# Performance work log

Measured on AMD Instinct MI355X. Metric: run time of the kernel, lower is better.

Reference implementation:

```python
import jax, jax.numpy as jnp
import numpy as np

SIGMA = 1.0  # init kwarg: Gaussian kernel width

B, P, F = 8192, 8192, 256


def setup_inputs() -> dict:
    key = jax.random.key(0)
    kx, kp = jax.random.split(key)
    x = jax.random.normal(kx, (B, F), dtype=jnp.float32)
    prototypes = jax.random.normal(kp, (P, F), dtype=jnp.float32)
    return {"x": x, "prototypes": prototypes}


def reference(x, prototypes):
    x_sq = jnp.sum(x * x, axis=-1, keepdims=True)            # [B,1]
    p_sq = jnp.sum(prototypes * prototypes, axis=-1)          # [P]
    cross = jnp.einsum('bf,pf->bp', x, prototypes)            # [B,P]
    d2 = jnp.maximum(x_sq + p_sq[None, :] - 2.0 * cross, 0.0)
    # NOTE: original takes .pow(0.5) -> euclidean NORM (despite variable name)
    dist = jnp.sqrt(d2)                                       # [B,P]
    denom = jnp.float32(2.0 * SIGMA ** 2)
    return jnp.exp(-dist / denom)
```

## Files before the change

### kernel.cpp

```cpp
#include <hip/hip_runtime.h>
#include <cstdint>
#include <cstddef>

#define B_ROWS 8192
#define P_ROWS 8192
#define FDIM   256

#define BM 128
#define BN 128
#define BK 64
#define NSTEP (FDIM / BK)

typedef __bf16  bf16x8  __attribute__((ext_vector_type(8)));
typedef float   floatx4 __attribute__((ext_vector_type(4)));

__device__ __forceinline__ unsigned short f2bf(float f) {
  unsigned int u = __float_as_uint(f);
  u += 0x7fffu + ((u >> 16) & 1u);
  return (unsigned short)(u >> 16);
}

__device__ __forceinline__ void async16(const void* g, void* l) {
  __builtin_amdgcn_global_load_lds(
      (const __attribute__((address_space(1))) void*)g,
      (__attribute__((address_space(3))) void*)l,
      16, 0, 0);
}

__global__ void __launch_bounds__(64) prep_kernel(
    const float* __restrict__ x, const float* __restrict__ p,
    unsigned short* __restrict__ xbf, unsigned short* __restrict__ pbf,
    float* __restrict__ x2, float* __restrict__ p2) {
  const int row  = blockIdx.x;
  const int lane = threadIdx.x;

  const float* src;
  unsigned short* dst;
  float* nrm;
  int r;
  if (row < B_ROWS) { src = x; dst = xbf; nrm = x2; r = row; }
  else              { src = p; dst = pbf; nrm = p2; r = row - B_ROWS; }

  const float4 v = *reinterpret_cast<const float4*>(src + (size_t)r * FDIM + lane * 4);
  float s = v.x * v.x + v.y * v.y + v.z * v.z + v.w * v.w;
  #pragma unroll
  for (int o = 32; o > 0; o >>= 1) s += __shfl_down(s, o);
  if (lane == 0) nrm[r] = s;

  ushort4 pk;
  pk.x = f2bf(v.x); pk.y = f2bf(v.y); pk.z = f2bf(v.z); pk.w = f2bf(v.w);
  *reinterpret_cast<ushort4*>(dst + (size_t)r * FDIM + lane * 4) = pk;
}

__global__ void __launch_bounds__(512, 4) gauss_kernel(
    const unsigned short* __restrict__ xbf, const unsigned short* __restrict__ pbf,
    const float* __restrict__ x2, const float* __restrict__ p2,
    float* __restrict__ out) {
  __shared__ __align__(16) unsigned short lds_a[2][BM * BK];
  __shared__ __align__(16) unsigned short lds_b[2][BN * BK];

  const int t    = threadIdx.x;
  const int lane = t & 63;
  const int w    = t >> 6;
  const int wr   = w >> 1;
  const int wc   = w & 1;
  const int lm   = lane & 15;
  const int q    = lane >> 4;
  const int sx   = lane & 7;

  const int f   = blockIdx.x;
  const int xcd = f & 7;
  const int idx = f >> 3;
  const int M0  = (xcd * 8 + (idx & 7)) * BM;
  const int N0  = (idx >> 3) * BN;

  unsigned int aOff[2], bOff[2], lOff[2];
  #pragma unroll
  for (int I = 0; I < 2; ++I) {
    const int L = I * 512 + t;
    const int r = L >> 3;
    const int c = L & 7;
    const int g = c ^ (r & 7);
    aOff[I] = (unsigned int)(((M0 + r) * FDIM + g * 8) * 2);
    const int pr = (r & 64) + 4 * (r & 15) + ((r >> 4) & 3);
    bOff[I] = (unsigned int)(((N0 + pr) * FDIM + g * 8) * 2);
    lOff[I] = (unsigned int)(L * 16);
  }
  const char* xB = (const char*)xbf;
  const char* pB = (const char*)pbf;

  floatx4 x2v[2];
  #pragma unroll
  for (int i = 0; i < 2; ++i)
    x2v[i] = *(const floatx4*)&x2[M0 + wr * 32 + i * 16 + q * 4];
  const floatx4 p2r = *(const floatx4*)&p2[N0 + wc * 64 + 4 * lm];

  #pragma unroll
  for (int I = 0; I < 2; ++I) async16(xB + aOff[I], (char*)&lds_a[0][0] + lOff[I]);
  #pragma unroll
  for (int I = 0; I < 2; ++I) async16(pB + bOff[I], (char*)&lds_b[0][0] + lOff[I]);
  __syncthreads();

  floatx4 acc[2][4] = {};

  #pragma unroll
  for (int s = 0; s < NSTEP; ++s) {
    const int b = s & 1;

    if (s + 1 < NSTEP) {
      const unsigned int ko = (unsigned int)((s + 1) * BK * 2);
      #pragma unroll
      for (int I = 0; I < 2; ++I)
        async16(xB + aOff[I] + ko, (char*)&lds_a[b ^ 1][0] + lOff[I]);
      #pragma unroll
      for (int I = 0; I < 2; ++I)
        async16(pB + bOff[I] + ko, (char*)&lds_b[b ^ 1][0] + lOff[I]);
    }

    #pragma unroll
    for (int kk = 0; kk < 2; ++kk) {
      const int slot = ((kk * 4 + q) ^ sx) * 8;
      bf16x8 af[2], bfr[4];
      #pragma unroll
      for (int i = 0; i < 2; ++i)
        af[i] = *(const bf16x8*)&lds_a[b][(wr * 32 + i * 16 + lm) * BK + slot];
      #pragma unroll
      for (int j = 0; j < 4; ++j)
        bfr[j] = *(const bf16x8*)&lds_b[b][(wc * 64 + j * 16 + lm) * BK + slot];
      #pragma unroll
      for (int i = 0; i < 2; ++i)
        #pragma unroll
        for (int j = 0; j < 4; ++j)
          acc[i][j] = __builtin_amdgcn_mfma_f32_16x16x32_bf16(af[i], bfr[j], acc[i][j], 0, 0, 0);
    }

    if (s + 1 < NSTEP) __syncthreads();
  }

  #pragma unroll
  for (int i = 0; i < 2; ++i) {
    #pragma unroll
    for (int v = 0; v < 4; ++v) {
      floatx4 res;
      #pragma unroll
      for (int j = 0; j < 4; ++j) {
        float d2 = x2v[i][v] + p2r[j] - 2.0f * acc[i][j][v];
        d2 = fmaxf(d2, 0.0f);
        res[j] = __expf(-0.5f * sqrtf(d2));
      }
      __builtin_nontemporal_store(
          res, (floatx4*)(out + (size_t)(M0 + wr * 32 + i * 16 + q * 4 + v) * P_ROWS
                          + N0 + wc * 64 + 4 * lm));
    }
  }
}

extern "C" void kernel_launch(void* const* d_in, const int* in_sizes, int n_in,
                              void* d_out, int out_size, void* d_ws, size_t ws_size,
                              hipStream_t stream) {
  const float* x = (const float*)d_in[0];
  const float* p = (const float*)d_in[1];
  float* out = (float*)d_out;

  char* ws = (char*)d_ws;
  unsigned short* xbf = (unsigned short*)ws;
  unsigned short* pbf = (unsigned short*)(ws + (size_t)B_ROWS * FDIM * 2);
  float* x2 = (float*)(ws + (size_t)(B_ROWS + P_ROWS) * FDIM * 2);
  float* p2 = x2 + B_ROWS;

  prep_kernel<<<dim3(B_ROWS + P_ROWS), dim3(64), 0, stream>>>(x, p, xbf, pbf, x2, p2);

  gauss_kernel<<<dim3((B_ROWS / BM) * (P_ROWS / BN)), dim3(512), 0, stream>>>(
      xbf, pbf, x2, p2, out);
}
```

Measured before the change: 311.3 us.

## Shrink GEMM tile to 64x128, drop double buffering, remap blocks, batch prep rows

The main kernel now uses 64x128 output tiles with 256 threads and a single LDS buffer, where it had 128x128 tiles, 512 threads and two buffers. Each K-step loads synchronously between two barriers. The block-to-tile mapping now groups blocks on each XCD by prototype column strips, and the prep kernel handles four rows per 256-thread block. The aim is more resident blocks and less LDS per block, but it gives up the overlap of loads with MFMA work and adds an extra barrier per step.

```diff
diff --git a/kernel.cpp b/kernel.cpp
--- a/kernel.cpp
+++ b/kernel.cpp
@@ -6,7 +6,7 @@
 #define P_ROWS 8192
 #define FDIM   256
 
-#define BM 128
+#define BM 64
 #define BN 128
 #define BK 64
 #define NSTEP (FDIM / BK)
@@ -27,12 +27,12 @@
       16, 0, 0);
 }
 
-__global__ void __launch_bounds__(64) prep_kernel(
+__global__ void __launch_bounds__(256) prep_kernel(
     const float* __restrict__ x, const float* __restrict__ p,
     unsigned short* __restrict__ xbf, unsigned short* __restrict__ pbf,
     float* __restrict__ x2, float* __restrict__ p2) {
-  const int row  = blockIdx.x;
-  const int lane = threadIdx.x;
+  const int row  = blockIdx.x * 4 + (threadIdx.x >> 6);
+  const int lane = threadIdx.x & 63;
 
   const float* src;
   unsigned short* dst;
@@ -52,12 +52,12 @@
   *reinterpret_cast<ushort4*>(dst + (size_t)r * FDIM + lane * 4) = pk;
 }
 
-__global__ void __launch_bounds__(512, 4) gauss_kernel(
+__global__ void __launch_bounds__(256, 4) gauss_kernel(
     const unsigned short* __restrict__ xbf, const unsigned short* __restrict__ pbf,
     const float* __restrict__ x2, const float* __restrict__ p2,
     float* __restrict__ out) {
-  __shared__ __align__(16) unsigned short lds_a[2][BM * BK];
-  __shared__ __align__(16) unsigned short lds_b[2][BN * BK];
+  __shared__ __align__(16) unsigned short lds_a[BM * BK];
+  __shared__ __align__(16) unsigned short lds_b[BN * BK];
 
   const int t    = threadIdx.x;
   const int lane = t & 63;
@@ -66,25 +66,33 @@
   const int wc   = w & 1;
   const int lm   = lane & 15;
   const int q    = lane >> 4;
-  const int sx   = lane & 7;
+  const int sx   = lm & 7;
 
   const int f   = blockIdx.x;
   const int xcd = f & 7;
   const int idx = f >> 3;
-  const int M0  = (xcd * 8 + (idx & 7)) * BM;
-  const int N0  = (idx >> 3) * BN;
+  const int bm  = idx & 127;
+  const int bn  = xcd * 8 + (idx >> 7);
+  const int M0  = bm * BM;
+  const int N0  = bn * BN;
 
-  unsigned int aOff[2], bOff[2], lOff[2];
+  unsigned int aOff[2], bOff[4];
   #pragma unroll
   for (int I = 0; I < 2; ++I) {
-    const int L = I * 512 + t;
+    const int L = I * 256 + t;
     const int r = L >> 3;
     const int c = L & 7;
     const int g = c ^ (r & 7);
     aOff[I] = (unsigned int)(((M0 + r) * FDIM + g * 8) * 2);
+  }
+  #pragma unroll
+  for (int I = 0; I < 4; ++I) {
+    const int L = I * 256 + t;
+    const int r = L >> 3;
+    const int c = L & 7;
+    const int g = c ^ (r & 7);
     const int pr = (r & 64) + 4 * (r & 15) + ((r >> 4) & 3);
     bOff[I] = (unsigned int)(((N0 + pr) * FDIM + g * 8) * 2);
-    lOff[I] = (unsigned int)(L * 16);
   }
   const char* xB = (const char*)xbf;
   const char* pB = (const char*)pbf;
@@ -95,27 +103,18 @@
     x2v[i] = *(const floatx4*)&x2[M0 + wr * 32 + i * 16 + q * 4];
   const floatx4 p2r = *(const floatx4*)&p2[N0 + wc * 64 + 4 * lm];
 
-  #pragma unroll
-  for (int I = 0; I < 2; ++I) async16(xB + aOff[I], (char*)&lds_a[0][0] + lOff[I]);
-  #pragma unroll
-  for (int I = 0; I < 2; ++I) async16(pB + bOff[I], (char*)&lds_b[0][0] + lOff[I]);
-  __syncthreads();
-
   floatx4 acc[2][4] = {};
 
-  #pragma unroll
   for (int s = 0; s < NSTEP; ++s) {
-    const int b = s & 1;
-
-    if (s + 1 < NSTEP) {
-      const unsigned int ko = (unsigned int)((s + 1) * BK * 2);
-      #pragma unroll
-      for (int I = 0; I < 2; ++I)
-        async16(xB + aOff[I] + ko, (char*)&lds_a[b ^ 1][0] + lOff[I]);
-      #pragma unroll
-      for (int I = 0; I < 2; ++I)
-        async16(pB + bOff[I] + ko, (char*)&lds_b[b ^ 1][0] + lOff[I]);
-    }
+    const unsigned int ko = (unsigned int)(s * (BK * 2));
+    __syncthreads();
+    #pragma unroll
+    for (int I = 0; I < 2; ++I)
+      async16(xB + aOff[I] + ko, (char*)lds_a + (unsigned int)((I * 256 + t) * 16));
+    #pragma unroll
+    for (int I = 0; I < 4; ++I)
+      async16(pB + bOff[I] + ko, (char*)lds_b + (unsigned int)((I * 256 + t) * 16));
+    __syncthreads();
 
     #pragma unroll
     for (int kk = 0; kk < 2; ++kk) {
@@ -123,18 +122,16 @@
       bf16x8 af[2], bfr[4];
       #pragma unroll
       for (int i = 0; i < 2; ++i)
-        af[i] = *(const bf16x8*)&lds_a[b][(wr * 32 + i * 16 + lm) * BK + slot];
+        af[i] = *(const bf16x8*)&lds_a[(wr * 32 + i * 16 + lm) * BK + slot];
       #pragma unroll
       for (int j = 0; j < 4; ++j)
-        bfr[j] = *(const bf16x8*)&lds_b[b][(wc * 64 + j * 16 + lm) * BK + slot];
+        bfr[j] = *(const bf16x8*)&lds_b[(wc * 64 + j * 16 + lm) * BK + slot];
       #pragma unroll
       for (int i = 0; i < 2; ++i)
         #pragma unroll
         for (int j = 0; j < 4; ++j)
           acc[i][j] = __builtin_amdgcn_mfma_f32_16x16x32_bf16(af[i], bfr[j], acc[i][j], 0, 0, 0);
     }
-
-    if (s + 1 < NSTEP) __syncthreads();
   }
 
   #pragma unroll
@@ -168,8 +165,9 @@
   float* x2 = (float*)(ws + (size_t)(B_ROWS + P_ROWS) * FDIM * 2);
   float* p2 = x2 + B_ROWS;
 
-  prep_kernel<<<dim3(B_ROWS + P_ROWS), dim3(64), 0, stream>>>(x, p, xbf, pbf, x2, p2);
+  prep_kernel<<<dim3((B_ROWS + P_ROWS) / 4), dim3(256), 0, stream>>>(
+      x, p, xbf, pbf, x2, p2);
 
-  gauss_kernel<<<dim3((B_ROWS / BM) * (P_ROWS / BN)), dim3(512), 0, stream>>>(
+  gauss_kernel<<<dim3((B_ROWS / BM) * (P_ROWS / BN)), dim3(256), 0, stream>>>(
       xbf, pbf, x2, p2, out);
 }
```

Measured after the change: 313.7 us. No clear change (+0.8%).
